# Kernel optimization log

Measured on AMD Instinct MI355X. Metric: run time of the kernel, lower is better.

## Reference

```python
import jax, jax.numpy as jnp
import numpy as np

A = 9            # cfg.anchors.num
K = 1000         # cfg.frcnn.nms.output_size
IOU_THR = 0.7    # cfg.frcnn.nms.iou
NEG = jnp.float32(-1e30)


def setup_inputs() -> dict:
    key = jax.random.key(0)
    ks = jax.random.split(key, 8)
    B, H, W, C = 1, 100, 152, 1024
    feat = jax.random.normal(ks[0], (B, H, W, C), jnp.float32)
    # conv kernels with small (0.01) std, matching typical RPN truncated-normal init
    w_cls = jax.random.normal(ks[1], (C, 2 * A), jnp.float32) * 0.01
    b_cls = jnp.zeros((2 * A,), jnp.float32)
    w_bbox = jax.random.normal(ks[2], (C, 4 * A), jnp.float32) * 0.01
    b_bbox = jnp.zeros((4 * A,), jnp.float32)
    img_sz = jnp.array([800.0, 1216.0], jnp.float32)
    N = B * H * W * A  # 136800 anchors, [x0, y0, x1, y1]
    cx = jax.random.uniform(ks[3], (N,), jnp.float32, 0.0, 800.0)
    cy = jax.random.uniform(ks[4], (N,), jnp.float32, 0.0, 1216.0)
    sh = jax.random.uniform(ks[5], (N,), jnp.float32, 16.0, 128.0)
    sw = jax.random.uniform(ks[6], (N,), jnp.float32, 16.0, 128.0)
    anchors = jnp.stack([cx - 0.5 * sh, cy - 0.5 * sw, cx + 0.5 * sh, cy + 0.5 * sw], axis=1)
    return {"rpn_feature": feat, "anchors": anchors, "img_sz": img_sz,
            "w_cls": w_cls, "b_cls": b_cls, "w_bbox": w_bbox, "b_bbox": b_bbox}


def convert_and_clip(anchors, pred, img_sz):
    # anchors [N,4]; decode deltas (tx pairs with h, ty with w, per original code)
    w = anchors[:, 3] - anchors[:, 1] + 1.0
    h = anchors[:, 2] - anchors[:, 0] + 1.0
    x = anchors[:, 0] + 0.5 * h
    y = anchors[:, 1] + 0.5 * w
    tx, ty, tw, th = pred[:, 0], pred[:, 1], pred[:, 2], pred[:, 3]
    x_pred = tx * h + x
    y_pred = ty * w + y
    w_pred = jnp.exp(tw) * w
    h_pred = jnp.exp(th) * h
    x0 = jnp.maximum(x_pred - 0.5 * h_pred, 0.0)
    x1 = jnp.minimum(x_pred + 0.5 * h_pred, img_sz[0])
    y0 = jnp.maximum(y_pred - 0.5 * w_pred, 0.0)
    y1 = jnp.minimum(y_pred + 0.5 * w_pred, img_sz[1])
    return jnp.stack([x0, y0, x1, y1], axis=1)


def greedy_nms(boxes, scores, k, iou_thr):
    # boxes [N,4] = [c0, c1, c2, c3]; IoU is symmetric in coord convention
    x0, y0, x1, y1 = boxes[:, 0], boxes[:, 1], boxes[:, 2], boxes[:, 3]
    areas = (x1 - x0) * (y1 - y0)

    def step(s, _):
        i = jnp.argmax(s)
        valid = s[i] > NEG * 0.5
        iw = jnp.maximum(jnp.minimum(x1, x1[i]) - jnp.maximum(x0, x0[i]), 0.0)
        ih = jnp.maximum(jnp.minimum(y1, y1[i]) - jnp.maximum(y0, y0[i]), 0.0)
        inter = iw * ih
        iou = inter / (areas + areas[i] - inter + 1e-9)
        s = jnp.where((iou >= iou_thr) & valid, NEG, s)
        s = s.at[i].set(NEG)
        return s, (i, valid)

    _, (idx, valid) = jax.lax.scan(step, scores, None, length=k)
    return idx, valid


def reference(rpn_feature, anchors, img_sz, w_cls, b_cls, w_bbox, b_bbox):
    # 1x1 convs == per-pixel GEMM
    cls_score = jnp.einsum('bhwc,co->bhwo', rpn_feature, w_cls) + b_cls       # [B,H,W,2A]
    cls_prob2 = jax.nn.softmax(cls_score.reshape(-1, 2), axis=-1)             # pairwise softmax
    cls_pred = jnp.argmax(cls_prob2, axis=-1)
    cls_prob = cls_prob2.reshape(cls_score.shape)
    bbox_pred = (jnp.einsum('bhwc,co->bhwo', rpn_feature, w_bbox) + b_bbox).reshape(-1, 4)
    fg = cls_prob[:, :, :, A:].reshape(-1)                                    # foreground scores
    boxes = convert_and_clip(anchors, bbox_pred, img_sz)                      # [N,4]
    idx, valid = greedy_nms(boxes, fg, K, IOU_THR)
    proposals = jnp.where(valid[:, None], boxes[idx], 0.0)                    # [K,4]
    return proposals, idx, cls_prob, cls_pred, bbox_pred
```

## Files before the change

kernel.cpp:

```cpp
#include <hip/hip_runtime.h>
#include <cstdint>
#include <cstddef>

#define NPOS   15200
#define NANCH  136800
#define KDIM   1024
#define NCLS   18
#define NBB    36
#define KS     4
#define KCH    (KDIM / KS)
#define KSTEP  64
#define MCAP   4096
#define NROW   2048
#define NWRD   32
#define TARGET_SEL 3072
#define KSEL   1000
#define HBINS  8192

typedef unsigned long long u64;

#define OFF_PROP    0
#define OFF_IDX     4000
#define OFF_CLSPROB 5000
#define OFF_CLSPRED 278600
#define OFF_BB      415400

struct Ctrl {
  int selCount;
  int bstar;
  int pad[14];
};

__device__ inline unsigned int fkey(float f) {
  unsigned int b = __float_as_uint(f);
  return (b & 0x80000000u) ? ~b : (b | 0x80000000u);
}

__global__ __launch_bounds__(256) void gemm2(const float* __restrict__ feat,
                                             const float* __restrict__ wcls,
                                             const float* __restrict__ wbb,
                                             double* __restrict__ diffPart,
                                             float* __restrict__ clsPart,
                                             float* __restrict__ bbPart) {
  __shared__ float  fS[64][67];
  __shared__ double wD[64][10];
  __shared__ float  wF[64][60];
  const int t = threadIdx.x;
  const int pos = t & 63;
  const int wv  = t >> 6;
  const int P0 = blockIdx.x * 64;
  const int k0 = blockIdx.y * KCH;

  double accd[9];
  float  accf[18];
#pragma unroll
  for (int c = 0; c < 9; ++c) accd[c] = 0.0;
#pragma unroll
  for (int c = 0; c < 18; ++c) accf[c] = 0.f;

  float4 fr[4];

  auto LOADF = [&](int kb) {
#pragma unroll
    for (int it = 0; it < 4; ++it) {
      int idx = it * 256 + t;
      int p = idx >> 4, q = idx & 15;
      int gp = P0 + p;
      fr[it] = make_float4(0.f, 0.f, 0.f, 0.f);
      if (gp < NPOS) fr[it] = *(const float4*)(feat + (size_t)gp * KDIM + kb + q * 4);
    }
  };
  auto WRITEF = [&]() {
#pragma unroll
    for (int it = 0; it < 4; ++it) {
      int idx = it * 256 + t;
      int p = idx >> 4, q = idx & 15;
      fS[p][q * 4 + 0] = fr[it].x; fS[p][q * 4 + 1] = fr[it].y;
      fS[p][q * 4 + 2] = fr[it].z; fS[p][q * 4 + 3] = fr[it].w;
    }
  };
  auto LOADW = [&](int kb) {
    for (int idx = t; idx < 64 * 18; idx += 256) {
      int k = idx / 18, c = idx % 18;
      wF[k][c] = wcls[(size_t)(kb + k) * NCLS + c];
    }
    for (int idx = t; idx < 64 * 36; idx += 256) {
      int k = idx / 36, c = idx % 36;
      wF[k][(c < 18) ? (20 + c) : (40 + (c - 18))] = wbb[(size_t)(kb + k) * NBB + c];
    }
    for (int idx = t; idx < 64 * 9; idx += 256) {
      int k = idx / 9, j = idx % 9;
      int cC = 9 + j, cD = cC ^ 1;
      wD[k][j] = (double)wcls[(size_t)(kb + k) * NCLS + cC] -
                 (double)wcls[(size_t)(kb + k) * NCLS + cD];
    }
  };

  LOADF(k0);
  WRITEF();
  LOADW(k0);
  __syncthreads();

  const int NSTEP = KCH / KSTEP;
  for (int s = 0; s < NSTEP; ++s) {
    if (s + 1 < NSTEP) LOADF(k0 + (s + 1) * KSTEP);
    if (wv == 0) {
#pragma unroll 4
      for (int kk = 0; kk < KSTEP; ++kk) {
        double f = (double)fS[pos][kk];
#pragma unroll
        for (int j = 0; j < 9; ++j) accd[j] += f * wD[kk][j];
      }
    } else {
      const int cb = (wv - 1) * 20;
#pragma unroll 4
      for (int kk = 0; kk < KSTEP; ++kk) {
        float f = fS[pos][kk];
#pragma unroll
        for (int c = 0; c < 18; ++c) accf[c] += f * wF[kk][cb + c];
      }
    }
    if (s + 1 < NSTEP) {
      __syncthreads();
      WRITEF();
      LOADW(k0 + (s + 1) * KSTEP);
      __syncthreads();
    }
  }

  int gp = P0 + pos;
  if (gp < NPOS) {
    if (wv == 0) {
      double* o = diffPart + ((size_t)blockIdx.y * NPOS + gp) * 9;
#pragma unroll
      for (int j = 0; j < 9; ++j) o[j] = accd[j];
    } else if (wv == 1) {
      float* o = clsPart + ((size_t)blockIdx.y * NPOS + gp) * NCLS;
#pragma unroll
      for (int c = 0; c < 18; ++c) o[c] = accf[c];
    } else {
      float* o = bbPart + ((size_t)blockIdx.y * NPOS + gp) * NBB + (wv - 2) * 18;
#pragma unroll
      for (int c = 0; c < 18; ++c) o[c] = accf[c];
    }
  }
}

__global__ __launch_bounds__(256) void epilogue(const double* __restrict__ diffPart, const float* __restrict__ clsPart,
                         const float* __restrict__ bbPart,
                         const float* __restrict__ bcls, const float* __restrict__ bbb,
                         const float* __restrict__ anchors, const float* __restrict__ imgsz,
                         float* __restrict__ out, double* __restrict__ dkeys,
                         float* __restrict__ bx0, float* __restrict__ by0,
                         float* __restrict__ bx1, float* __restrict__ by1,
                         float* __restrict__ bar, int* __restrict__ hist) {
  __shared__ int hS[HBINS];
  const int t = threadIdx.x;
  for (int i = t; i < HBINS; i += 256) hS[i] = 0;
  __syncthreads();

  int n = blockIdx.x * 256 + t;
  if (n < NANCH) {
    int pos = n / 9, j = n % 9;
    int cA = 2 * j, cB = 2 * j + 1, cC = 9 + j, cD = cC ^ 1;
    float sA = bcls[cA], sB = bcls[cB];
#pragma unroll
    for (int ks = 0; ks < KS; ++ks) {
      const float* pp = clsPart + ((size_t)ks * NPOS + pos) * NCLS;
      sA += pp[cA]; sB += pp[cB];
    }
    double d = (double)bcls[cC] - (double)bcls[cD];
#pragma unroll
    for (int ks = 0; ks < KS; ++ks)
      d += diffPart[((size_t)ks * NPOS + pos) * 9 + j];

    out[OFF_CLSPROB + (size_t)pos * 18 + cA] = 1.0f / (1.0f + expf(sB - sA));
    out[OFF_CLSPROB + (size_t)pos * 18 + cB] = 1.0f / (1.0f + expf(sA - sB));
    out[OFF_CLSPRED + n] = (sB > sA) ? 1.0f : 0.0f;
    dkeys[n] = d;
    atomicAdd(&hS[fkey((float)d) >> 19], 1);

    float tb[4];
#pragma unroll
    for (int m = 0; m < 4; ++m) {
      float s = bbb[4 * j + m];
#pragma unroll
      for (int ks = 0; ks < KS; ++ks)
        s += bbPart[((size_t)ks * NPOS + pos) * NBB + 4 * j + m];
      tb[m] = s;
      out[OFF_BB + (size_t)n * 4 + m] = s;
    }
    float4 a = *(const float4*)(anchors + (size_t)n * 4);
    float w = a.w - a.y + 1.0f;
    float h = a.z - a.x + 1.0f;
    float x = a.x + 0.5f * h;
    float y = a.y + 0.5f * w;
    float xp = tb[0] * h + x;
    float yp = tb[1] * w + y;
    float wp = expf(tb[2]) * w;
    float hp = expf(tb[3]) * h;
    float X0 = fmaxf(xp - 0.5f * hp, 0.f);
    float X1 = fminf(xp + 0.5f * hp, imgsz[0]);
    float Y0 = fmaxf(yp - 0.5f * wp, 0.f);
    float Y1 = fminf(yp + 0.5f * wp, imgsz[1]);
    bx0[n] = X0; by0[n] = Y0; bx1[n] = X1; by1[n] = Y1;
    bar[n] = (X1 - X0) * (Y1 - Y0);
  }

  __syncthreads();
  for (int i = t; i < HBINS; i += 256) {
    int v = hS[i];
    if (v) atomicAdd(&hist[i], v);
  }
}

__global__ void scank(const int* __restrict__ hist, Ctrl* __restrict__ ctrl) {
  __shared__ int hS[HBINS];
  __shared__ int cS[256];
  int t = threadIdx.x;
  for (int i = t; i < HBINS; i += 256) hS[i] = hist[i];
  __syncthreads();
  int s = 0;
  for (int b = 0; b < 32; ++b) s += hS[t * 32 + b];
  cS[t] = s;
  __syncthreads();
  if (t == 0) {
    int acc = 0;
    for (int cb = 255; cb >= 0; --cb) {
      int cs = cS[cb];
      if (acc + cs >= TARGET_SEL || acc + cs > MCAP) {
        int bstar = cb * 32;
        for (int b = cb * 32 + 31; b >= cb * 32; --b) {
          int h = hS[b];
          if (acc + h > MCAP) { bstar = b + 1; break; }
          acc += h;
          if (acc >= TARGET_SEL) { bstar = b; break; }
        }
        ctrl->bstar = bstar;
        return;
      }
      acc += cs;
    }
    ctrl->bstar = 0;
  }
}

__global__ void compactk(const double* __restrict__ dkeys, Ctrl* __restrict__ ctrl,
                         int* __restrict__ sel) {
  int n = blockIdx.x * blockDim.x + threadIdx.x;
  if (n >= NANCH) return;
  unsigned int u = fkey((float)dkeys[n]);
  if ((int)(u >> 19) >= ctrl->bstar) {
    int slot = atomicAdd(&ctrl->selCount, 1);
    if (slot < MCAP) sel[slot] = n;
  }
}

__global__ __launch_bounds__(256) void rankk(const double* __restrict__ dkeys,
                                             const int* __restrict__ sel,
                                             const Ctrl* __restrict__ ctrl,
                                             int* __restrict__ rank) {
  int C = ctrl->selCount; if (C > MCAP) C = MCAP;
  if ((int)(blockIdx.x << 8) >= C || (int)(blockIdx.y << 8) >= C) return;
  __shared__ double kS[256];
  __shared__ int    iS[256];
  const int t = threadIdx.x;
  int j = blockIdx.y * 256 + t;
  if (j < C) { int n = sel[j]; kS[t] = dkeys[n]; iS[t] = n; }
  else       { kS[t] = -1.0e300; iS[t] = NANCH + j; }
  int i = blockIdx.x * 256 + t;
  double ki; int ii;
  if (i < C) { int n = sel[i]; ki = dkeys[n]; ii = n; }
  else       { ki = -1.0e300; ii = NANCH + i; }
  __syncthreads();
  int cnt = 0;
#pragma unroll 8
  for (int q = 0; q < 256; ++q) {
    double kq = kS[q]; int iq = iS[q];
    cnt += (int)((kq > ki) || (kq == ki && iq < ii));
  }
  atomicAdd(&rank[i], cnt);
}

__global__ __launch_bounds__(256) void scatterk(const int* __restrict__ sel,
                                                const Ctrl* __restrict__ ctrl,
                                                const int* __restrict__ rank,
                                                int* __restrict__ sidx,
                                                float* __restrict__ sx0, float* __restrict__ sy0,
                                                float* __restrict__ sx1, float* __restrict__ sy1,
                                                float* __restrict__ sar,
                                                const float* __restrict__ bx0, const float* __restrict__ by0,
                                                const float* __restrict__ bx1, const float* __restrict__ by1,
                                                const float* __restrict__ bar) {
  int i = blockIdx.x * 256 + threadIdx.x;
  if (i >= MCAP) return;
  int C = ctrl->selCount;
  if (C > MCAP) C = MCAP;
  if (i < C) {
    int r = rank[i];
    if (r < 0 || r >= MCAP) return;
    int n = sel[i];
    sidx[r] = n;
    sx0[r] = bx0[n]; sy0[r] = by0[n]; sx1[r] = bx1[n]; sy1[r] = by1[n]; sar[r] = bar[n];
  } else {
    sidx[i] = 0x7FFFFFFF;
    sx0[i] = 0.f; sy0[i] = 0.f; sx1[i] = 0.f; sy1[i] = 0.f; sar[i] = 0.f;
  }
}

__global__ __launch_bounds__(256) void iouk2(const float* __restrict__ sx0, const float* __restrict__ sy0,
                                             const float* __restrict__ sx1, const float* __restrict__ sy1,
                                             const float* __restrict__ sar,
                                             u64* __restrict__ mask) {
  __shared__ float X0[NROW], Y0[NROW], X1[NROW], Y1[NROW], AR[NROW];
  int t = threadIdx.x;
  for (int i = t; i < NROW; i += 256) {
    X0[i] = sx0[i]; Y0[i] = sy0[i]; X1[i] = sx1[i]; Y1[i] = sy1[i]; AR[i] = sar[i];
  }
  __syncthreads();
  int r0 = blockIdx.x * 16;
  for (int task = t; task < 16 * NWRD; task += 256) {
    int r = r0 + (task >> 5);
    int w = task & 31;
    float x0r = X0[r], y0r = Y0[r], x1r = X1[r], y1r = Y1[r], arr = AR[r];
    u64 bits = 0ull;
#pragma unroll 16
    for (int jj = 0; jj < 64; ++jj) {
      int jc = (w << 6) + jj;
      float iw = fminf(x1r, X1[jc]) - fmaxf(x0r, X0[jc]);
      iw = fmaxf(iw, 0.f);
      float ih = fminf(y1r, Y1[jc]) - fmaxf(y0r, Y0[jc]);
      ih = fmaxf(ih, 0.f);
      float inter = iw * ih;
      float iou = inter / (AR[jc] + arr - inter + 1e-9f);
      bits |= ((u64)(iou >= 0.7f)) << jj;
    }
    mask[(size_t)r * NWRD + w] = bits;
  }
}

__global__ __launch_bounds__(64) void nmsk2(const u64* __restrict__ mask,
                                            const int* __restrict__ sidx,
                                            const float* __restrict__ sx0, const float* __restrict__ sy0,
                                            const float* __restrict__ sx1, const float* __restrict__ sy1,
                                            const float* __restrict__ sar,
                                            const Ctrl* __restrict__ ctrl,
                                            float* __restrict__ out) {
  __shared__ int keptPos[KSEL];
  const int lane = threadIdx.x;
  const int h = lane >> 5, m = lane & 31;
  int C = ctrl->selCount; if (C > MCAP) C = MCAP;
  int kept = 0;
  u64 sup = 0;
  const int nwin = min((C + 63) >> 6, NROW >> 6);

  u64 bufA[32], bufB[32], dgA = 0, dgB = 0;

  auto ISSUE = [&](u64* buf, u64& dg, int w) {
    const u64* base = mask + ((size_t)(w * 64 + h * 32) * NWRD + m);
#pragma unroll
    for (int j = 0; j < 32; ++j) buf[j] = base[(size_t)j * NWRD];
    dg = mask[((size_t)(w * 64 + lane)) * NWRD + w];
  };

  auto PROCW = [&](u64* buf, u64 dg, int w) {
    u64 swin = __shfl(sup, w);
    int rem = C - w * 64;
    u64 vmask = (rem >= 64) ? ~0ull : ((1ull << rem) - 1);
    u64 cand = (~swin) & vmask;
    u64 keep = 0;
    if (cand) {
      u64 gt = (lane == 63) ? 0ull : (~0ull << (lane + 1));
      bool own = (cand >> lane) & 1;
      u64 bad = __ballot(own && ((dg & cand & gt) != 0ull));
      if (bad == 0ull) {
        keep = cand;
      } else {
        u64 cur = cand;
        for (int j = 0; j < 64; ++j) {
          if ((cur >> j) & 1) {
            keep |= 1ull << j;
            u64 dj = __shfl(dg, j);
            u64 gtj = (j == 63) ? 0ull : (~0ull << (j + 1));
            cur &= ~(dj & gtj);
          }
        }
      }
    }
    int pc = __popcll(keep);
    int need = KSEL - kept;
    while (pc > need) { keep &= ~(1ull << (63 - __clzll(keep))); --pc; }
    if ((keep >> lane) & 1) {
      int p = kept + __popcll(keep & ((1ull << lane) - 1ull));
      keptPos[p] = w * 64 + lane;
    }
    u64 orv = 0;
    u64 kmh = h ? (keep >> 32) : (keep & 0xffffffffull);
#pragma unroll
    for (int j = 0; j < 32; ++j)
      if ((kmh >> j) & 1) orv |= buf[j];
    orv |= __shfl_xor(orv, 32);
    sup |= orv;
    kept += pc;
  };

  if (nwin > 0) {
    ISSUE(bufA, dgA, 0);
    int w = 0;
    while (w < nwin && kept < KSEL) {
      if (w + 1 < nwin) ISSUE(bufB, dgB, w + 1);
      PROCW(bufA, dgA, w); ++w;
      if (w >= nwin || kept >= KSEL) break;
      if (w + 1 < nwin) ISSUE(bufA, dgA, w + 1);
      PROCW(bufB, dgB, w); ++w;
    }
  }

  for (int r = NROW; r < C && kept < KSEL; ++r) {
    float x0 = sx0[r], y0 = sy0[r], x1 = sx1[r], y1 = sy1[r], ar = sar[r];
    bool supr = false;
    for (int b = lane; b < kept; b += 64) {
      int kp = keptPos[b];
      float iw = fminf(x1, sx1[kp]) - fmaxf(x0, sx0[kp]);
      iw = fmaxf(iw, 0.f);
      float ih = fminf(y1, sy1[kp]) - fmaxf(y0, sy0[kp]);
      ih = fmaxf(ih, 0.f);
      float inter = iw * ih;
      float iou = inter / (sar[kp] + ar - inter + 1e-9f);
      if (iou >= 0.7f) supr = true;
    }
    if (__ballot(supr) != 0ull) continue;
    if (lane == 0) keptPos[kept] = r;
    ++kept;
  }

  __syncthreads();
  for (int q = lane; q < KSEL; q += 64) {
    if (q < kept) {
      int kp = keptPos[q];
      int n = sidx[kp];
      out[OFF_PROP + 4 * q + 0] = sx0[kp];
      out[OFF_PROP + 4 * q + 1] = sy0[kp];
      out[OFF_PROP + 4 * q + 2] = sx1[kp];
      out[OFF_PROP + 4 * q + 3] = sy1[kp];
      out[OFF_IDX + q] = (float)n;
    } else {
      out[OFF_PROP + 4 * q + 0] = 0.f;
      out[OFF_PROP + 4 * q + 1] = 0.f;
      out[OFF_PROP + 4 * q + 2] = 0.f;
      out[OFF_PROP + 4 * q + 3] = 0.f;
      out[OFF_IDX + q] = 0.f;
    }
  }
}

__global__ void badws(float* out) {
  if (threadIdx.x == 0 && blockIdx.x == 0) out[0] = 1.0e8f;
}

extern "C" void kernel_launch(void* const* d_in, const int* in_sizes, int n_in,
                              void* d_out, int out_size, void* d_ws, size_t ws_size,
                              hipStream_t stream) {
  (void)in_sizes; (void)n_in; (void)out_size;
  const float* feat    = (const float*)d_in[0];
  const float* anchors = (const float*)d_in[1];
  const float* imgsz   = (const float*)d_in[2];
  const float* wcls    = (const float*)d_in[3];
  const float* bcls    = (const float*)d_in[4];
  const float* wbb     = (const float*)d_in[5];
  const float* bbb     = (const float*)d_in[6];
  float* out = (float*)d_out;
  char* ws = (char*)d_ws;

  const size_t o_diff   = 0;
  const size_t o_cls    = o_diff + (size_t)KS * NPOS * 9 * 8;
  const size_t o_bb     = o_cls + (size_t)KS * NPOS * NCLS * 4;
  const size_t o_dkeys  = o_bb + (size_t)KS * NPOS * NBB * 4;
  const size_t o_bx0    = o_dkeys + (size_t)NANCH * 8;
  const size_t o_by0    = o_bx0 + (size_t)NANCH * 4;
  const size_t o_bx1    = o_by0 + (size_t)NANCH * 4;
  const size_t o_by1    = o_bx1 + (size_t)NANCH * 4;
  const size_t o_bar    = o_by1 + (size_t)NANCH * 4;
  const size_t o_hist   = o_bar + (size_t)NANCH * 4;
  const size_t o_ctrl   = o_hist + (size_t)HBINS * 4;
  const size_t o_rank   = o_ctrl + 256;
  const size_t o_sel    = o_rank + (size_t)MCAP * 4;
  const size_t o_sidx   = o_sel + (size_t)MCAP * 4;
  const size_t o_sx0    = o_sidx + (size_t)MCAP * 4;
  const size_t o_sy0    = o_sx0 + (size_t)MCAP * 4;
  const size_t o_sx1    = o_sy0 + (size_t)MCAP * 4;
  const size_t o_sy1    = o_sx1 + (size_t)MCAP * 4;
  const size_t o_sar    = o_sy1 + (size_t)MCAP * 4;
  const size_t o_mask   = o_sar + (size_t)MCAP * 4;
  const size_t need     = o_mask + (size_t)NROW * NWRD * 8;

  if (ws_size < need) {
    badws<<<dim3(1), dim3(64), 0, stream>>>(out);
    return;
  }

  double* diffPart = (double*)(ws + o_diff);
  float*  clsPart  = (float*)(ws + o_cls);
  float*  bbPart   = (float*)(ws + o_bb);
  double* dkeys    = (double*)(ws + o_dkeys);
  float*  bx0      = (float*)(ws + o_bx0);
  float*  by0      = (float*)(ws + o_by0);
  float*  bx1      = (float*)(ws + o_bx1);
  float*  by1      = (float*)(ws + o_by1);
  float*  bar      = (float*)(ws + o_bar);
  int*    hist     = (int*)(ws + o_hist);
  Ctrl*   ctrl     = (Ctrl*)(ws + o_ctrl);
  int*    rank     = (int*)(ws + o_rank);
  int*    sel      = (int*)(ws + o_sel);
  int*    sidx     = (int*)(ws + o_sidx);
  float*  sx0      = (float*)(ws + o_sx0);
  float*  sy0      = (float*)(ws + o_sy0);
  float*  sx1      = (float*)(ws + o_sx1);
  float*  sy1      = (float*)(ws + o_sy1);
  float*  sar      = (float*)(ws + o_sar);
  u64*    mask     = (u64*)(ws + o_mask);

  hipMemsetAsync(ws + o_hist, 0, (size_t)HBINS * 4 + 256 + (size_t)MCAP * 4, stream);

  gemm2<<<dim3(238, KS), dim3(256), 0, stream>>>(feat, wcls, wbb, diffPart, clsPart, bbPart);
  epilogue<<<dim3((NANCH + 255) / 256), dim3(256), 0, stream>>>(
      diffPart, clsPart, bbPart, bcls, bbb, anchors, imgsz, out, dkeys, bx0, by0, bx1, by1, bar, hist);
  scank<<<dim3(1), dim3(256), 0, stream>>>(hist, ctrl);
  compactk<<<dim3((NANCH + 255) / 256), dim3(256), 0, stream>>>(dkeys, ctrl, sel);
  rankk<<<dim3(MCAP / 256, MCAP / 256), dim3(256), 0, stream>>>(dkeys, sel, ctrl, rank);
  scatterk<<<dim3(MCAP / 256), dim3(256), 0, stream>>>(sel, ctrl, rank, sidx,
                                                       sx0, sy0, sx1, sy1, sar,
                                                       bx0, by0, bx1, by1, bar);
  iouk2<<<dim3(NROW / 16), dim3(256), 0, stream>>>(sx0, sy0, sx1, sy1, sar, mask);
  nmsk2<<<dim3(1), dim3(64), 0, stream>>>(mask, sidx, sx0, sy0, sx1, sy1, sar, ctrl, out);
}
```

Baseline: 195.4 us.

## Retile RPN GEMM to 512-position register tiles and use ballot-based compaction

The feature GEMM kernel now gives each thread 8 positions instead of 1. Features are staged into a swizzled transposed shared tile of 512 positions by 32 k, and weights are read as vector loads and reused across the 8 positions. The K split rises to 8, which raises the number of partial sums the epilogue must reduce. The launch shrinks to a grid of 30x8 blocks with heavy register use, which risks low occupancy and less latency hiding, and the previous register prefetch double-buffering is dropped. Compaction now uses a wave ballot and prefix count with one atomic per block instead of one atomic per selected element.

```diff
diff --git a/kernel.cpp b/kernel.cpp
--- a/kernel.cpp
+++ b/kernel.cpp
@@ -7,9 +7,10 @@
 #define KDIM   1024
 #define NCLS   18
 #define NBB    36
-#define KS     4
+#define KS     8
 #define KCH    (KDIM / KS)
-#define KSTEP  64
+#define KSTEP  32
+#define MTILE  512
 #define MCAP   4096
 #define NROW   2048
 #define NWRD   32
@@ -36,112 +37,130 @@
   return (b & 0x80000000u) ? ~b : (b | 0x80000000u);
 }
 
-__global__ __launch_bounds__(256) void gemm2(const float* __restrict__ feat,
-                                             const float* __restrict__ wcls,
-                                             const float* __restrict__ wbb,
-                                             double* __restrict__ diffPart,
-                                             float* __restrict__ clsPart,
-                                             float* __restrict__ bbPart) {
-  __shared__ float  fS[64][67];
-  __shared__ double wD[64][10];
-  __shared__ float  wF[64][60];
+__global__ __launch_bounds__(256, 1) void gemm3(const float* __restrict__ feat,
+                                                const float* __restrict__ wcls,
+                                                const float* __restrict__ wbb,
+                                                double* __restrict__ diffPart,
+                                                float* __restrict__ clsPart,
+                                                float* __restrict__ bbPart) {
+  __shared__ __align__(16) float  fS[KSTEP * 512];
+  __shared__ __align__(16) float  wF[KSTEP][72];
+  __shared__ __align__(16) double wD[KSTEP][12];
   const int t = threadIdx.x;
-  const int pos = t & 63;
-  const int wv  = t >> 6;
-  const int P0 = blockIdx.x * 64;
+  const int lane = t & 63;
+  const int wv   = t >> 6;
+  const int P0 = blockIdx.x * MTILE;
   const int k0 = blockIdx.y * KCH;
 
-  double accd[9];
-  float  accf[18];
-#pragma unroll
-  for (int c = 0; c < 9; ++c) accd[c] = 0.0;
-#pragma unroll
-  for (int c = 0; c < 18; ++c) accf[c] = 0.f;
-
-  float4 fr[4];
-
-  auto LOADF = [&](int kb) {
-#pragma unroll
-    for (int it = 0; it < 4; ++it) {
-      int idx = it * 256 + t;
-      int p = idx >> 4, q = idx & 15;
+  double accd[8][9];
+  float  accf[8][18];
+#pragma unroll
+  for (int p = 0; p < 8; ++p) {
+#pragma unroll
+    for (int j = 0; j < 9; ++j) accd[p][j] = 0.0;
+#pragma unroll
+    for (int c = 0; c < 18; ++c) accf[p][c] = 0.f;
+  }
+
+  auto STAGE = [&](int kb) {
+#pragma unroll
+    for (int j = 0; j < 16; ++j) {
+      int idx = j * 256 + t;
+      int p = idx >> 3, q = idx & 7;
       int gp = P0 + p;
-      fr[it] = make_float4(0.f, 0.f, 0.f, 0.f);
-      if (gp < NPOS) fr[it] = *(const float4*)(feat + (size_t)gp * KDIM + kb + q * 4);
-    }
-  };
-  auto WRITEF = [&]() {
-#pragma unroll
-    for (int it = 0; it < 4; ++it) {
-      int idx = it * 256 + t;
-      int p = idx >> 4, q = idx & 15;
-      fS[p][q * 4 + 0] = fr[it].x; fS[p][q * 4 + 1] = fr[it].y;
-      fS[p][q * 4 + 2] = fr[it].z; fS[p][q * 4 + 3] = fr[it].w;
-    }
-  };
-  auto LOADW = [&](int kb) {
-    for (int idx = t; idx < 64 * 18; idx += 256) {
+      float4 v = make_float4(0.f, 0.f, 0.f, 0.f);
+      if (gp < NPOS) v = *(const float4*)(feat + (size_t)gp * KDIM + kb + q * 4);
+      const float vv[4] = {v.x, v.y, v.z, v.w};
+#pragma unroll
+      for (int i = 0; i < 4; ++i) {
+        int kk = q * 4 + i;
+        int swz = ((kk >> 2) & 7) << 2;
+        fS[kk * 512 + (p ^ swz)] = vv[i];
+      }
+    }
+    for (int idx = t; idx < KSTEP * 18; idx += 256) {
       int k = idx / 18, c = idx % 18;
       wF[k][c] = wcls[(size_t)(kb + k) * NCLS + c];
     }
-    for (int idx = t; idx < 64 * 36; idx += 256) {
+    for (int idx = t; idx < KSTEP * 36; idx += 256) {
       int k = idx / 36, c = idx % 36;
-      wF[k][(c < 18) ? (20 + c) : (40 + (c - 18))] = wbb[(size_t)(kb + k) * NBB + c];
-    }
-    for (int idx = t; idx < 64 * 9; idx += 256) {
-      int k = idx / 9, j = idx % 9;
-      int cC = 9 + j, cD = cC ^ 1;
-      wD[k][j] = (double)wcls[(size_t)(kb + k) * NCLS + cC] -
-                 (double)wcls[(size_t)(kb + k) * NCLS + cD];
+      wF[k][(c < 18) ? (24 + c) : (48 + (c - 18))] = wbb[(size_t)(kb + k) * NBB + c];
+    }
+    for (int idx = t; idx < KSTEP * 9; idx += 256) {
+      int k = idx / 9, jj = idx % 9;
+      int cC = 9 + jj, cD = cC ^ 1;
+      wD[k][jj] = (double)wcls[(size_t)(kb + k) * NCLS + cC] -
+                  (double)wcls[(size_t)(kb + k) * NCLS + cD];
     }
   };
 
-  LOADF(k0);
-  WRITEF();
-  LOADW(k0);
-  __syncthreads();
-
-  const int NSTEP = KCH / KSTEP;
-  for (int s = 0; s < NSTEP; ++s) {
-    if (s + 1 < NSTEP) LOADF(k0 + (s + 1) * KSTEP);
+  for (int s = 0; s < KCH / KSTEP; ++s) {
+    if (s) __syncthreads();
+    STAGE(k0 + s * KSTEP);
+    __syncthreads();
     if (wv == 0) {
-#pragma unroll 4
+#pragma unroll 2
       for (int kk = 0; kk < KSTEP; ++kk) {
-        double f = (double)fS[pos][kk];
-#pragma unroll
-        for (int j = 0; j < 9; ++j) accd[j] += f * wD[kk][j];
+        int swz = ((kk >> 2) & 7) << 2;
+        const float4 fa = *(const float4*)&fS[kk * 512 + ((lane * 4) ^ swz)];
+        const float4 fb = *(const float4*)&fS[kk * 512 + ((256 + lane * 4) ^ swz)];
+        const double f[8] = {(double)fa.x, (double)fa.y, (double)fa.z, (double)fa.w,
+                             (double)fb.x, (double)fb.y, (double)fb.z, (double)fb.w};
+        const double2 w01 = *(const double2*)&wD[kk][0];
+        const double2 w23 = *(const double2*)&wD[kk][2];
+        const double2 w45 = *(const double2*)&wD[kk][4];
+        const double2 w67 = *(const double2*)&wD[kk][6];
+        const double  w8  = wD[kk][8];
+        const double w[9] = {w01.x, w01.y, w23.x, w23.y, w45.x, w45.y, w67.x, w67.y, w8};
+#pragma unroll
+        for (int p = 0; p < 8; ++p)
+#pragma unroll
+          for (int j = 0; j < 9; ++j) accd[p][j] += f[p] * w[j];
       }
     } else {
-      const int cb = (wv - 1) * 20;
-#pragma unroll 4
+      const int cb = (wv - 1) * 24;
+#pragma unroll 2
       for (int kk = 0; kk < KSTEP; ++kk) {
-        float f = fS[pos][kk];
-#pragma unroll
-        for (int c = 0; c < 18; ++c) accf[c] += f * wF[kk][cb + c];
+        int swz = ((kk >> 2) & 7) << 2;
+        const float4 fa = *(const float4*)&fS[kk * 512 + ((lane * 4) ^ swz)];
+        const float4 fb = *(const float4*)&fS[kk * 512 + ((256 + lane * 4) ^ swz)];
+        const float f[8] = {fa.x, fa.y, fa.z, fa.w, fb.x, fb.y, fb.z, fb.w};
+        const float4 w0 = *(const float4*)&wF[kk][cb + 0];
+        const float4 w1 = *(const float4*)&wF[kk][cb + 4];
+        const float4 w2 = *(const float4*)&wF[kk][cb + 8];
+        const float4 w3 = *(const float4*)&wF[kk][cb + 12];
+        const float4 w4 = *(const float4*)&wF[kk][cb + 16];
+        const float w[18] = {w0.x, w0.y, w0.z, w0.w, w1.x, w1.y, w1.z, w1.w,
+                             w2.x, w2.y, w2.z, w2.w, w3.x, w3.y, w3.z, w3.w,
+                             w4.x, w4.y};
+#pragma unroll
+        for (int p = 0; p < 8; ++p)
+#pragma unroll
+          for (int c = 0; c < 18; ++c) accf[p][c] += f[p] * w[c];
       }
     }
-    if (s + 1 < NSTEP) {
-      __syncthreads();
-      WRITEF();
-      LOADW(k0 + (s + 1) * KSTEP);
-      __syncthreads();
-    }
-  }
-
-  int gp = P0 + pos;
-  if (gp < NPOS) {
+  }
+
+  int plocal[8];
+#pragma unroll
+  for (int i = 0; i < 4; ++i) { plocal[i] = lane * 4 + i; plocal[4 + i] = 256 + lane * 4 + i; }
+
+#pragma unroll
+  for (int i = 0; i < 8; ++i) {
+    int gp = P0 + plocal[i];
+    if (gp >= NPOS) continue;
     if (wv == 0) {
       double* o = diffPart + ((size_t)blockIdx.y * NPOS + gp) * 9;
 #pragma unroll
-      for (int j = 0; j < 9; ++j) o[j] = accd[j];
+      for (int j = 0; j < 9; ++j) o[j] = accd[i][j];
     } else if (wv == 1) {
       float* o = clsPart + ((size_t)blockIdx.y * NPOS + gp) * NCLS;
 #pragma unroll
-      for (int c = 0; c < 18; ++c) o[c] = accf[c];
+      for (int c = 0; c < 18; ++c) o[c] = accf[i][c];
     } else {
       float* o = bbPart + ((size_t)blockIdx.y * NPOS + gp) * NBB + (wv - 2) * 18;
 #pragma unroll
-      for (int c = 0; c < 18; ++c) o[c] = accf[c];
+      for (int c = 0; c < 18; ++c) o[c] = accf[i][c];
     }
   }
 }
@@ -245,13 +264,31 @@
   }
 }
 
-__global__ void compactk(const double* __restrict__ dkeys, Ctrl* __restrict__ ctrl,
-                         int* __restrict__ sel) {
-  int n = blockIdx.x * blockDim.x + threadIdx.x;
-  if (n >= NANCH) return;
-  unsigned int u = fkey((float)dkeys[n]);
-  if ((int)(u >> 19) >= ctrl->bstar) {
-    int slot = atomicAdd(&ctrl->selCount, 1);
+__global__ __launch_bounds__(256) void compactk(const double* __restrict__ dkeys, Ctrl* __restrict__ ctrl,
+                                                int* __restrict__ sel) {
+  __shared__ int wofs[4];
+  __shared__ int base;
+  const int t = threadIdx.x;
+  const int lane = t & 63, wv = t >> 6;
+  int n = blockIdx.x * 256 + t;
+  bool pick = false;
+  if (n < NANCH) {
+    unsigned int u = fkey((float)dkeys[n]);
+    pick = ((int)(u >> 19) >= ctrl->bstar);
+  }
+  u64 b = __ballot(pick);
+  int wpre = __popcll(b & ((lane == 0) ? 0ull : (~0ull >> (64 - lane))));
+  if (lane == 0) wofs[wv] = __popcll(b);
+  __syncthreads();
+  if (t == 0) {
+    int c0 = wofs[0], c1 = wofs[1], c2 = wofs[2], c3 = wofs[3];
+    int tot = c0 + c1 + c2 + c3;
+    wofs[0] = 0; wofs[1] = c0; wofs[2] = c0 + c1; wofs[3] = c0 + c1 + c2;
+    base = tot ? atomicAdd(&ctrl->selCount, tot) : 0;
+  }
+  __syncthreads();
+  if (pick) {
+    int slot = base + wofs[wv] + wpre;
     if (slot < MCAP) sel[slot] = n;
   }
 }
@@ -522,7 +559,8 @@
 
   hipMemsetAsync(ws + o_hist, 0, (size_t)HBINS * 4 + 256 + (size_t)MCAP * 4, stream);
 
-  gemm2<<<dim3(238, KS), dim3(256), 0, stream>>>(feat, wcls, wbb, diffPart, clsPart, bbPart);
+  gemm3<<<dim3((NPOS + MTILE - 1) / MTILE, KS), dim3(256), 0, stream>>>(
+      feat, wcls, wbb, diffPart, clsPart, bbPart);
   epilogue<<<dim3((NANCH + 255) / 256), dim3(256), 0, stream>>>(
       diffPart, clsPart, bbPart, bcls, bbb, anchors, imgsz, out, dkeys, bx0, by0, bx1, by1, bar, hist);
   scank<<<dim3(1), dim3(256), 0, stream>>>(hist, ctrl);
```

Result: slower. 200.9 us (+2.8%).
